# Kernel tuning notes

Measured on AMD Instinct MI355X. Metric: run time of the kernel, lower is better.

## Reference

```python
import jax, jax.numpy as jnp
import numpy as np

SIGMA = 1.0
EPSILON = 5.0
ALPHA = 5.0
CUTOFF = 2.5
N_ATOMS = 262144
N_PAIRS = 8388608
BOX = 5.0


def setup_inputs() -> dict:
    key = jax.random.key(0)
    k1, k2 = jax.random.split(key, 2)
    positions = jax.random.uniform(k1, (N_ATOMS, 3), dtype=jnp.float32) * BOX
    mapping = jax.random.randint(k2, (2, N_PAIRS), 0, N_ATOMS)
    shifts = jnp.zeros((N_PAIRS, 3), dtype=jnp.float32)
    cell = jnp.eye(3, dtype=jnp.float32) * BOX
    return {"positions": positions, "cell": cell, "shifts": shifts, "mapping": mapping}


def reference(positions, cell, shifts, mapping):
    i, j = mapping[0], mapping[1]
    # displacement for each neighbor pair (gather), including PBC shift vectors
    dr_vec = positions[j] - positions[i] + shifts @ cell            # [E,3]
    distances = jnp.linalg.norm(dr_vec, axis=-1)                    # [E]
    safe_dist = jnp.where(distances > 1e-10, distances, 1.0)

    # Morse pair energy: eps*(1 - exp(-alpha*(r - sigma)))^2 - eps
    e = jnp.exp(-ALPHA * (distances - SIGMA))
    pair_energies = EPSILON * (1.0 - e) ** 2 - EPSILON
    mask = (distances < CUTOFF) & (distances > 1e-10)
    pair_energies = jnp.where(mask, pair_energies, 0.0)

    energy = 0.5 * jnp.sum(pair_energies)

    # per-atom energy decomposition (scatter-add)
    atom_energies = jnp.zeros((positions.shape[0],), dtype=positions.dtype)
    atom_energies = atom_energies.at[i].add(0.5 * pair_energies)
    atom_energies = atom_energies.at[j].add(0.5 * pair_energies)

    # Morse pair force magnitude: -dE/dr = -2*alpha*eps*e*(1 - e)
    pair_forces = -2.0 * ALPHA * EPSILON * e * (1.0 - e)
    pair_forces = jnp.where(mask, pair_forces, 0.0)
    force_vectors = (pair_forces / safe_dist)[:, None] * dr_vec     # [E,3]

    forces = jnp.zeros_like(positions)
    forces = forces.at[i].add(-force_vectors)
    forces = forces.at[j].add(force_vectors)

    # virial stress: -sum_pairs outer(dr, f) / volume
    stress_per_pair = jnp.einsum("ei,ej->eij", dr_vec, force_vectors)  # [E,3,3]
    volume = jnp.abs(jnp.linalg.det(cell))
    stress = -jnp.sum(stress_per_pair, axis=0) / volume

    return energy, atom_energies, forces, stress
```

## Files before the change

### kernel.cpp

```cpp
#include <hip/hip_runtime.h>

#define NATOMS 262144
#define NPAIRS 8388608
#define THREADS 1024
#define PPT 4
#define BLKP (THREADS * PPT)
#define NBLK2 (NPAIRS / BLKP)
#define NBUCK  512
#define NREG   (8 * NBUCK)
#define CAP    3400

#define C_SIGMA   1.0f
#define C_EPS     5.0f
#define C_ALPHA   5.0f
#define C_CUTOFF  2.5f

#define OUT_E 0
#define OUT_AE 1
#define OUT_F (1 + NATOMS)
#define OUT_S (1 + 4 * NATOMS)

#define POS4_OFF  ((size_t)0)
#define CUR_OFF   ((size_t)4 * NATOMS)
#define PART_OFF  (CUR_OFF + NREG)
#define REC_OFF   (PART_OFF + (size_t)NBLK2 * 8)
#define WS_DWORDS (REC_OFF + (size_t)NREG * CAP * 4)

typedef int   i32x4 __attribute__((ext_vector_type(4)));
typedef float f32x4 __attribute__((ext_vector_type(4)));

__device__ __forceinline__ int xcc_id() {
    return (int)(__builtin_amdgcn_s_getreg((3 << 11) | 20) & 7);
}

__device__ __forceinline__ unsigned bf16_rne(float f) {
    unsigned u = __float_as_uint(f);
    return (u + 0x7FFFu + ((u >> 16) & 1u)) >> 16;
}

__device__ __forceinline__ unsigned l2_fetch_add(unsigned* p, unsigned v) {
    return __hip_atomic_fetch_add(p, v, __ATOMIC_RELAXED, __HIP_MEMORY_SCOPE_WORKGROUP);
}

__global__ __launch_bounds__(256) void prep_kernel(
    const float* __restrict__ pos, unsigned* __restrict__ ws)
{
    const int a = blockIdx.x * blockDim.x + threadIdx.x;
    float4* pos4 = reinterpret_cast<float4*>(ws + POS4_OFF);
    if (a < NATOMS)
        pos4[a] = make_float4(pos[3 * a + 0], pos[3 * a + 1], pos[3 * a + 2], 0.0f);
    if (a < NREG)
        ws[CUR_OFF + a] = 0u;
}

__global__ __launch_bounds__(THREADS) void morse_fused(
    const float* __restrict__ cell, const float* __restrict__ shifts,
    const int* __restrict__ mi, const int* __restrict__ mj,
    unsigned* __restrict__ ws)
{
    __shared__ unsigned cnt[NBUCK];
    __shared__ unsigned bases[NBUCK];

    const float4* __restrict__ pos4 = reinterpret_cast<const float4*>(ws + POS4_OFF);
    const int t    = threadIdx.x;
    const int blk  = blockIdx.x;
    const int base = (blk * THREADS + t) * PPT;
    const int xcc  = xcc_id();
    unsigned* __restrict__ cur = ws + CUR_OFF + (size_t)xcc * NBUCK;
    uint4* __restrict__ recs = reinterpret_cast<uint4*>(ws + REC_OFF)
                             + (size_t)xcc * NBUCK * CAP;

    if (t < NBUCK) cnt[t] = 0u;
    __syncthreads();

    const float c00 = cell[0], c01 = cell[1], c02 = cell[2];
    const float c10 = cell[3], c11 = cell[4], c12 = cell[5];
    const float c20 = cell[6], c21 = cell[7], c22 = cell[8];

    const i32x4 i4 = __builtin_nontemporal_load(reinterpret_cast<const i32x4*>(mi + base));
    const i32x4 j4 = __builtin_nontemporal_load(reinterpret_cast<const i32x4*>(mj + base));
    const f32x4* shp = reinterpret_cast<const f32x4*>(shifts + (size_t)base * 3);
    const f32x4 s_a = __builtin_nontemporal_load(shp + 0);
    const f32x4 s_b = __builtin_nontemporal_load(shp + 1);
    const f32x4 s_c = __builtin_nontemporal_load(shp + 2);

    const int   ii[4] = { i4.x, i4.y, i4.z, i4.w };
    const int   jj[4] = { j4.x, j4.y, j4.z, j4.w };
    const float sh[12] = { s_a.x, s_a.y, s_a.z, s_a.w,
                           s_b.x, s_b.y, s_b.z, s_b.w,
                           s_c.x, s_c.y, s_c.z, s_c.w };

    float e_acc = 0.0f;
    float sxx = 0, syy = 0, szz = 0, sxy = 0, sxz = 0, syz = 0;

    bool  act[4];
    float vh[4], vx[4], vy[4], vz[4];
    unsigned offi[4], offj[4];

#pragma unroll
    for (int k = 0; k < PPT; ++k) {
        const int i = ii[k], j = jj[k];
        const float sx = sh[3 * k + 0], sy = sh[3 * k + 1], sz = sh[3 * k + 2];
        const float4 pi = pos4[i];
        const float4 pj = pos4[j];
        const float dx = pj.x - pi.x + sx * c00 + sy * c10 + sz * c20;
        const float dy = pj.y - pi.y + sx * c01 + sy * c11 + sz * c21;
        const float dz = pj.z - pi.z + sx * c02 + sy * c12 + sz * c22;
        const float r  = sqrtf(dx * dx + dy * dy + dz * dz);
        const bool active = (r < C_CUTOFF) && (r > 1e-10f);
        act[k] = active;
        float he = 0.0f, fx = 0.0f, fy = 0.0f, fz = 0.0f;
        if (active) {
            const float ex = __expf(-C_ALPHA * (r - C_SIGMA));
            const float om = 1.0f - ex;
            const float pe = C_EPS * om * om - C_EPS;
            const float tt = (-2.0f * C_ALPHA * C_EPS * ex * om) / r;
            fx = tt * dx; fy = tt * dy; fz = tt * dz;
            he = 0.5f * pe;
            e_acc += pe;
            sxx += fx * dx; syy += fy * dy; szz += fz * dz;
            sxy += fx * dy; sxz += fx * dz; syz += fy * dz;
            offi[k] = atomicAdd(&cnt[i >> 9], 1u);
            offj[k] = atomicAdd(&cnt[j >> 9], 1u);
        }
        vh[k] = he; vx[k] = fx; vy[k] = fy; vz[k] = fz;
    }

    __syncthreads();

    if (t < NBUCK) {
        const unsigned n = cnt[t];
        bases[t] = n ? l2_fetch_add(&cur[t], n) : 0u;
    }
    __syncthreads();

#pragma unroll
    for (int k = 0; k < PPT; ++k) {
        if (act[k]) {
            const unsigned hb = bf16_rne(vh[k]) << 16;
            const int a_i = ii[k], a_j = jj[k];
            const int bi = a_i >> 9, bj = a_j >> 9;
            const unsigned si = bases[bi] + offi[k];
            const unsigned sj = bases[bj] + offj[k];
            if (si < CAP) {
                uint4 r;
                r.x = (unsigned)(a_i & 511) | hb;
                r.y = __float_as_uint(-vx[k]);
                r.z = __float_as_uint(-vy[k]);
                r.w = __float_as_uint(-vz[k]);
                recs[(size_t)bi * CAP + si] = r;
            }
            if (sj < CAP) {
                uint4 r;
                r.x = (unsigned)(a_j & 511) | hb;
                r.y = __float_as_uint(vx[k]);
                r.z = __float_as_uint(vy[k]);
                r.w = __float_as_uint(vz[k]);
                recs[(size_t)bj * CAP + sj] = r;
            }
        }
    }

#pragma unroll
    for (int off = 32; off > 0; off >>= 1) {
        e_acc += __shfl_down(e_acc, off);
        sxx += __shfl_down(sxx, off); syy += __shfl_down(syy, off);
        szz += __shfl_down(szz, off); sxy += __shfl_down(sxy, off);
        sxz += __shfl_down(sxz, off); syz += __shfl_down(syz, off);
    }
    __shared__ float red[16][7];
    const int lane = t & 63, wid = t >> 6;
    if (lane == 0) {
        red[wid][0] = e_acc;
        red[wid][1] = sxx; red[wid][2] = syy; red[wid][3] = szz;
        red[wid][4] = sxy; red[wid][5] = sxz; red[wid][6] = syz;
    }
    __syncthreads();
    if (t < 7) {
        float a = 0.0f;
#pragma unroll
        for (int w = 0; w < 16; ++w) a += red[w][t];
        float* pf = reinterpret_cast<float*>(ws + PART_OFF) + (size_t)blk * 8;
        pf[t] = a;
    }
}

__global__ __launch_bounds__(THREADS) void morse_accum(
    const unsigned* __restrict__ ws, const float* __restrict__ cell,
    float* __restrict__ out)
{
    const int b = blockIdx.x;
    const int t = threadIdx.x;
    __shared__ float acc[512 * 5];
    for (int l = t; l < 512 * 5; l += THREADS) acc[l] = 0.0f;
    __syncthreads();

    const uint4* recbase = reinterpret_cast<const uint4*>(ws + REC_OFF);
#pragma unroll
    for (int x = 0; x < 8; ++x) {
        const int reg = x * NBUCK + b;
        unsigned n = ws[CUR_OFF + reg];
        if (n > CAP) n = CAP;
        const uint4* recs = recbase + (size_t)reg * CAP;
        for (unsigned r = t; r < n; r += THREADS) {
            const uint4 v = recs[r];
            const int idx = (int)(v.x & 511u) * 5;
            atomicAdd(&acc[idx + 0], __uint_as_float(v.x & 0xFFFF0000u));
            atomicAdd(&acc[idx + 1], __uint_as_float(v.y));
            atomicAdd(&acc[idx + 2], __uint_as_float(v.z));
            atomicAdd(&acc[idx + 3], __uint_as_float(v.w));
        }
    }
    __syncthreads();

    for (int l = t; l < 2048; l += THREADS) {
        if (l < 512) {
            out[OUT_AE + b * 512 + l] = acc[l * 5];
        } else {
            const int fl = l - 512;
            out[OUT_F + (size_t)b * 1536 + fl] = acc[(fl / 3) * 5 + 1 + fl % 3];
        }
    }

    if (b == 0) {
        const float* pf = reinterpret_cast<const float*>(ws + PART_OFF);
        float a[7] = {0, 0, 0, 0, 0, 0, 0};
        for (int r = t; r < NBLK2; r += THREADS) {
            const float* p = pf + (size_t)r * 8;
#pragma unroll
            for (int c = 0; c < 7; ++c) a[c] += p[c];
        }
#pragma unroll
        for (int off = 32; off > 0; off >>= 1) {
#pragma unroll
            for (int c = 0; c < 7; ++c) a[c] += __shfl_down(a[c], off);
        }
        __shared__ float red[16][7];
        const int lane = t & 63, wid = t >> 6;
        if (lane == 0) {
#pragma unroll
            for (int c = 0; c < 7; ++c) red[wid][c] = a[c];
        }
        __syncthreads();
        if (t == 0) {
            float acc7[7];
#pragma unroll
            for (int c = 0; c < 7; ++c) {
                float s = 0.0f;
#pragma unroll
                for (int w = 0; w < 16; ++w) s += red[w][c];
                acc7[c] = s;
            }
            const float c00 = cell[0], c01 = cell[1], c02 = cell[2];
            const float c10 = cell[3], c11 = cell[4], c12 = cell[5];
            const float c20 = cell[6], c21 = cell[7], c22 = cell[8];
            const float det = c00 * (c11 * c22 - c12 * c21)
                            - c01 * (c10 * c22 - c12 * c20)
                            + c02 * (c10 * c21 - c11 * c20);
            const float s = -1.0f / fabsf(det);
            out[OUT_E] = 0.5f * acc7[0];
            float* st = out + OUT_S;
            st[0] = s * acc7[1]; st[4] = s * acc7[2]; st[8] = s * acc7[3];
            st[1] = s * acc7[4]; st[3] = s * acc7[4];
            st[2] = s * acc7[5]; st[6] = s * acc7[5];
            st[5] = s * acc7[6]; st[7] = s * acc7[6];
        }
    }
}

__global__ __launch_bounds__(256) void zero_out_kernel(float* __restrict__ out, int n) {
    int idx = blockIdx.x * blockDim.x + threadIdx.x;
    if (idx < n) out[idx] = 0.0f;
}

__global__ __launch_bounds__(256) void morse_pairs_direct(
    const float* __restrict__ pos, const float* __restrict__ cell,
    const float* __restrict__ shifts, const int* __restrict__ mi,
    const int* __restrict__ mj, float* __restrict__ out)
{
    float* atom_e = out + OUT_AE;
    float* forces = out + OUT_F;
    float* stress = out + OUT_S;
    const float c00 = cell[0], c01 = cell[1], c02 = cell[2];
    const float c10 = cell[3], c11 = cell[4], c12 = cell[5];
    const float c20 = cell[6], c21 = cell[7], c22 = cell[8];
    const float det = c00*(c11*c22-c12*c21) - c01*(c10*c22-c12*c20) + c02*(c10*c21-c11*c20);
    const float inv_vol = 1.0f / fabsf(det);
    const int tid = blockIdx.x * blockDim.x + threadIdx.x;
    const int base = tid * 4;
    const i32x4 i4 = *reinterpret_cast<const i32x4*>(mi + base);
    const i32x4 j4 = *reinterpret_cast<const i32x4*>(mj + base);
    const f32x4* shp = reinterpret_cast<const f32x4*>(shifts + (size_t)base * 3);
    const f32x4 s_a = shp[0], s_b = shp[1], s_c = shp[2];
    const int idx_i[4] = { i4.x, i4.y, i4.z, i4.w };
    const int idx_j[4] = { j4.x, j4.y, j4.z, j4.w };
    const float sh[12] = { s_a.x, s_a.y, s_a.z, s_a.w,
                           s_b.x, s_b.y, s_b.z, s_b.w,
                           s_c.x, s_c.y, s_c.z, s_c.w };
    float e_acc = 0, sxx = 0, syy = 0, szz = 0, sxy = 0, sxz = 0, syz = 0;
#pragma unroll
    for (int k = 0; k < 4; ++k) {
        const int i = idx_i[k], j = idx_j[k];
        const float sx = sh[3*k], sy = sh[3*k+1], sz = sh[3*k+2];
        const float dx = pos[3*j]   - pos[3*i]   + sx*c00 + sy*c10 + sz*c20;
        const float dy = pos[3*j+1] - pos[3*i+1] + sx*c01 + sy*c11 + sz*c21;
        const float dz = pos[3*j+2] - pos[3*i+2] + sx*c02 + sy*c12 + sz*c22;
        const float r = sqrtf(dx*dx + dy*dy + dz*dz);
        if (r < C_CUTOFF && r > 1e-10f) {
            const float ex = __expf(-C_ALPHA * (r - C_SIGMA));
            const float om = 1.0f - ex;
            const float pe = C_EPS * om * om - C_EPS;
            const float t  = (-2.0f * C_ALPHA * C_EPS * ex * om) / r;
            const float fx = t*dx, fy = t*dy, fz = t*dz;
            e_acc += pe;
            sxx += fx*dx; syy += fy*dy; szz += fz*dz;
            sxy += fx*dy; sxz += fx*dz; syz += fy*dz;
            const float he = 0.5f * pe;
            atomicAdd(atom_e + i, he);        atomicAdd(atom_e + j, he);
            atomicAdd(forces + 3*i + 0, -fx); atomicAdd(forces + 3*j + 0, fx);
            atomicAdd(forces + 3*i + 1, -fy); atomicAdd(forces + 3*j + 1, fy);
            atomicAdd(forces + 3*i + 2, -fz); atomicAdd(forces + 3*j + 2, fz);
        }
    }
#pragma unroll
    for (int off = 32; off > 0; off >>= 1) {
        e_acc += __shfl_down(e_acc, off);
        sxx += __shfl_down(sxx, off); syy += __shfl_down(syy, off);
        szz += __shfl_down(szz, off); sxy += __shfl_down(sxy, off);
        sxz += __shfl_down(sxz, off); syz += __shfl_down(syz, off);
    }
    if ((threadIdx.x & 63) == 0) {
        atomicAdd(out + OUT_E, 0.5f * e_acc);
        const float s = -inv_vol;
        atomicAdd(stress + 0, s*sxx); atomicAdd(stress + 4, s*syy);
        atomicAdd(stress + 8, s*szz);
        atomicAdd(stress + 1, s*sxy); atomicAdd(stress + 3, s*sxy);
        atomicAdd(stress + 2, s*sxz); atomicAdd(stress + 6, s*sxz);
        atomicAdd(stress + 5, s*syz); atomicAdd(stress + 7, s*syz);
    }
}

extern "C" void kernel_launch(void* const* d_in, const int* in_sizes, int n_in,
                              void* d_out, int out_size, void* d_ws, size_t ws_size,
                              hipStream_t stream) {
    const float* pos    = (const float*)d_in[0];
    const float* cell   = (const float*)d_in[1];
    const float* shifts = (const float*)d_in[2];
    const int*   map    = (const int*)d_in[3];
    float* out = (float*)d_out;

    if (ws_size >= WS_DWORDS * 4) {
        unsigned* ws = (unsigned*)d_ws;
        prep_kernel<<<NATOMS / 256, 256, 0, stream>>>(pos, ws);
        morse_fused<<<NBLK2, THREADS, 0, stream>>>(cell, shifts, map, map + NPAIRS, ws);
        morse_accum<<<NBUCK, THREADS, 0, stream>>>(ws, cell, out);
    } else {
        zero_out_kernel<<<(out_size + 255) / 256, 256, 0, stream>>>(out, out_size);
        morse_pairs_direct<<<NPAIRS / 1024, 256, 0, stream>>>(
            pos, cell, shifts, map, map + NPAIRS, out);
    }
}
```

Baseline: 418.9 us.

## Compress scatter records to 8 bytes with bf16 forces and recompute energy

Each bucketed scatter record shrinks from 16 to 8 bytes. Force components are now stored as bf16, and the per-atom energy is no longer stored. A 2-bit branch code is kept instead, and the accumulate kernel rebuilds the energy from the force magnitude by solving the Morse quadratic. This halves record write and read traffic between the two kernels. The pair kernel also moves from 1024 to 512 threads per block. The cost is lower force precision (bf16) and an energy rebuilt from rounded forces, so accuracy may degrade, especially near the branch boundaries.

```diff
diff --git a/kernel.cpp b/kernel.cpp
--- a/kernel.cpp
+++ b/kernel.cpp
@@ -2,10 +2,11 @@
 
 #define NATOMS 262144
 #define NPAIRS 8388608
-#define THREADS 1024
+#define FTHREADS 512
 #define PPT 4
-#define BLKP (THREADS * PPT)
+#define BLKP (FTHREADS * PPT)
 #define NBLK2 (NPAIRS / BLKP)
+#define ATHREADS 1024
 #define NBUCK  512
 #define NREG   (8 * NBUCK)
 #define CAP    3400
@@ -24,7 +25,7 @@
 #define CUR_OFF   ((size_t)4 * NATOMS)
 #define PART_OFF  (CUR_OFF + NREG)
 #define REC_OFF   (PART_OFF + (size_t)NBLK2 * 8)
-#define WS_DWORDS (REC_OFF + (size_t)NREG * CAP * 4)
+#define WS_DWORDS (REC_OFF + (size_t)NREG * CAP * 2)
 
 typedef int   i32x4 __attribute__((ext_vector_type(4)));
 typedef float f32x4 __attribute__((ext_vector_type(4)));
@@ -36,6 +37,9 @@
 __device__ __forceinline__ unsigned bf16_rne(float f) {
     unsigned u = __float_as_uint(f);
     return (u + 0x7FFFu + ((u >> 16) & 1u)) >> 16;
+}
+__device__ __forceinline__ float bf16_to_f(unsigned h) {
+    return __uint_as_float(h << 16);
 }
 
 __device__ __forceinline__ unsigned l2_fetch_add(unsigned* p, unsigned v) {
@@ -53,7 +57,7 @@
         ws[CUR_OFF + a] = 0u;
 }
 
-__global__ __launch_bounds__(THREADS) void morse_fused(
+__global__ __launch_bounds__(FTHREADS) void morse_fused(
     const float* __restrict__ cell, const float* __restrict__ shifts,
     const int* __restrict__ mi, const int* __restrict__ mj,
     unsigned* __restrict__ ws)
@@ -64,13 +68,13 @@
     const float4* __restrict__ pos4 = reinterpret_cast<const float4*>(ws + POS4_OFF);
     const int t    = threadIdx.x;
     const int blk  = blockIdx.x;
-    const int base = (blk * THREADS + t) * PPT;
+    const int base = (blk * FTHREADS + t) * PPT;
     const int xcc  = xcc_id();
     unsigned* __restrict__ cur = ws + CUR_OFF + (size_t)xcc * NBUCK;
-    uint4* __restrict__ recs = reinterpret_cast<uint4*>(ws + REC_OFF)
+    uint2* __restrict__ recs = reinterpret_cast<uint2*>(ws + REC_OFF)
                              + (size_t)xcc * NBUCK * CAP;
 
-    if (t < NBUCK) cnt[t] = 0u;
+    cnt[t] = 0u;
     __syncthreads();
 
     const float c00 = cell[0], c01 = cell[1], c02 = cell[2];
@@ -94,7 +98,8 @@
     float sxx = 0, syy = 0, szz = 0, sxy = 0, sxz = 0, syz = 0;
 
     bool  act[4];
-    float vh[4], vx[4], vy[4], vz[4];
+    unsigned code[4];
+    float vx[4], vy[4], vz[4];
     unsigned offi[4], offj[4];
 
 #pragma unroll
@@ -109,26 +114,27 @@
         const float r  = sqrtf(dx * dx + dy * dy + dz * dz);
         const bool active = (r < C_CUTOFF) && (r > 1e-10f);
         act[k] = active;
-        float he = 0.0f, fx = 0.0f, fy = 0.0f, fz = 0.0f;
+        float fx = 0.0f, fy = 0.0f, fz = 0.0f;
+        unsigned cd = 0;
         if (active) {
             const float ex = __expf(-C_ALPHA * (r - C_SIGMA));
             const float om = 1.0f - ex;
             const float pe = C_EPS * om * om - C_EPS;
             const float tt = (-2.0f * C_ALPHA * C_EPS * ex * om) / r;
             fx = tt * dx; fy = tt * dy; fz = tt * dz;
-            he = 0.5f * pe;
+            cd = (ex >= 1.0f) ? 2u : (ex >= 0.5f ? 1u : 0u);
             e_acc += pe;
             sxx += fx * dx; syy += fy * dy; szz += fz * dz;
             sxy += fx * dy; sxz += fx * dz; syz += fy * dz;
             offi[k] = atomicAdd(&cnt[i >> 9], 1u);
             offj[k] = atomicAdd(&cnt[j >> 9], 1u);
         }
-        vh[k] = he; vx[k] = fx; vy[k] = fy; vz[k] = fz;
-    }
-
-    __syncthreads();
-
-    if (t < NBUCK) {
+        code[k] = cd; vx[k] = fx; vy[k] = fy; vz[k] = fz;
+    }
+
+    __syncthreads();
+
+    {
         const unsigned n = cnt[t];
         bases[t] = n ? l2_fetch_add(&cur[t], n) : 0u;
     }
@@ -137,25 +143,21 @@
 #pragma unroll
     for (int k = 0; k < PPT; ++k) {
         if (act[k]) {
-            const unsigned hb = bf16_rne(vh[k]) << 16;
+            const unsigned cd9 = code[k] << 9;
             const int a_i = ii[k], a_j = jj[k];
             const int bi = a_i >> 9, bj = a_j >> 9;
             const unsigned si = bases[bi] + offi[k];
             const unsigned sj = bases[bj] + offj[k];
             if (si < CAP) {
-                uint4 r;
-                r.x = (unsigned)(a_i & 511) | hb;
-                r.y = __float_as_uint(-vx[k]);
-                r.z = __float_as_uint(-vy[k]);
-                r.w = __float_as_uint(-vz[k]);
+                uint2 r;
+                r.x = (unsigned)(a_i & 511) | cd9 | (bf16_rne(-vz[k]) << 16);
+                r.y = bf16_rne(-vx[k]) | (bf16_rne(-vy[k]) << 16);
                 recs[(size_t)bi * CAP + si] = r;
             }
             if (sj < CAP) {
-                uint4 r;
-                r.x = (unsigned)(a_j & 511) | hb;
-                r.y = __float_as_uint(vx[k]);
-                r.z = __float_as_uint(vy[k]);
-                r.w = __float_as_uint(vz[k]);
+                uint2 r;
+                r.x = (unsigned)(a_j & 511) | cd9 | (bf16_rne(vz[k]) << 16);
+                r.y = bf16_rne(vx[k]) | (bf16_rne(vy[k]) << 16);
                 recs[(size_t)bj * CAP + sj] = r;
             }
         }
@@ -168,7 +170,7 @@
         szz += __shfl_down(szz, off); sxy += __shfl_down(sxy, off);
         sxz += __shfl_down(sxz, off); syz += __shfl_down(syz, off);
     }
-    __shared__ float red[16][7];
+    __shared__ float red[8][7];
     const int lane = t & 63, wid = t >> 6;
     if (lane == 0) {
         red[wid][0] = e_acc;
@@ -179,41 +181,57 @@
     if (t < 7) {
         float a = 0.0f;
 #pragma unroll
-        for (int w = 0; w < 16; ++w) a += red[w][t];
+        for (int w = 0; w < 8; ++w) a += red[w][t];
         float* pf = reinterpret_cast<float*>(ws + PART_OFF) + (size_t)blk * 8;
         pf[t] = a;
     }
 }
 
-__global__ __launch_bounds__(THREADS) void morse_accum(
+__global__ __launch_bounds__(ATHREADS) void morse_accum(
     const unsigned* __restrict__ ws, const float* __restrict__ cell,
     float* __restrict__ out)
 {
     const int b = blockIdx.x;
     const int t = threadIdx.x;
     __shared__ float acc[512 * 5];
-    for (int l = t; l < 512 * 5; l += THREADS) acc[l] = 0.0f;
-    __syncthreads();
-
-    const uint4* recbase = reinterpret_cast<const uint4*>(ws + REC_OFF);
+    for (int l = t; l < 512 * 5; l += ATHREADS) acc[l] = 0.0f;
+    __syncthreads();
+
+    const uint2* recbase = reinterpret_cast<const uint2*>(ws + REC_OFF);
 #pragma unroll
     for (int x = 0; x < 8; ++x) {
         const int reg = x * NBUCK + b;
         unsigned n = ws[CUR_OFF + reg];
         if (n > CAP) n = CAP;
-        const uint4* recs = recbase + (size_t)reg * CAP;
-        for (unsigned r = t; r < n; r += THREADS) {
-            const uint4 v = recs[r];
+        const uint2* recs = recbase + (size_t)reg * CAP;
+        for (unsigned r = t; r < n; r += ATHREADS) {
+            const uint2 v = recs[r];
             const int idx = (int)(v.x & 511u) * 5;
-            atomicAdd(&acc[idx + 0], __uint_as_float(v.x & 0xFFFF0000u));
-            atomicAdd(&acc[idx + 1], __uint_as_float(v.y));
-            atomicAdd(&acc[idx + 2], __uint_as_float(v.z));
-            atomicAdd(&acc[idx + 3], __uint_as_float(v.w));
-        }
-    }
-    __syncthreads();
-
-    for (int l = t; l < 2048; l += THREADS) {
+            const unsigned cd = (v.x >> 9) & 3u;
+            const float fz = bf16_to_f(v.x >> 16);
+            const float fx = bf16_to_f(v.y & 0xFFFFu);
+            const float fy = bf16_to_f(v.y >> 16);
+            const float fmag = sqrtf(fx * fx + fy * fy + fz * fz);
+            const float c = fmag * (1.0f / (2.0f * C_ALPHA * C_EPS));
+            float e;
+            if (cd == 2u) {
+                e = 0.5f * (1.0f + sqrtf(1.0f + 4.0f * c));
+            } else {
+                const float s = sqrtf(fmaxf(1.0f - 4.0f * c, 0.0f));
+                e = (cd == 1u) ? 0.5f * (1.0f + s) : 0.5f * (1.0f - s);
+            }
+            const float om = 1.0f - e;
+            const float he = 0.5f * (C_EPS * om * om - C_EPS);
+
+            atomicAdd(&acc[idx + 0], he);
+            atomicAdd(&acc[idx + 1], fx);
+            atomicAdd(&acc[idx + 2], fy);
+            atomicAdd(&acc[idx + 3], fz);
+        }
+    }
+    __syncthreads();
+
+    for (int l = t; l < 2048; l += ATHREADS) {
         if (l < 512) {
             out[OUT_AE + b * 512 + l] = acc[l * 5];
         } else {
@@ -225,7 +243,7 @@
     if (b == 0) {
         const float* pf = reinterpret_cast<const float*>(ws + PART_OFF);
         float a[7] = {0, 0, 0, 0, 0, 0, 0};
-        for (int r = t; r < NBLK2; r += THREADS) {
+        for (int r = t; r < NBLK2; r += ATHREADS) {
             const float* p = pf + (size_t)r * 8;
 #pragma unroll
             for (int c = 0; c < 7; ++c) a[c] += p[c];
@@ -352,8 +370,8 @@
     if (ws_size >= WS_DWORDS * 4) {
         unsigned* ws = (unsigned*)d_ws;
         prep_kernel<<<NATOMS / 256, 256, 0, stream>>>(pos, ws);
-        morse_fused<<<NBLK2, THREADS, 0, stream>>>(cell, shifts, map, map + NPAIRS, ws);
-        morse_accum<<<NBUCK, THREADS, 0, stream>>>(ws, cell, out);
+        morse_fused<<<NBLK2, FTHREADS, 0, stream>>>(cell, shifts, map, map + NPAIRS, ws);
+        morse_accum<<<NBUCK, ATHREADS, 0, stream>>>(ws, cell, out);
     } else {
         zero_out_kernel<<<(out_size + 255) / 256, 256, 0, stream>>>(out, out_size);
         morse_pairs_direct<<<NPAIRS / 1024, 256, 0, stream>>>(
```

Measured after the change: 415.9 us. Within noise of the previous version (-0.7%).
